# Kernel tuning notes

Measured on AMD Instinct MI355X. Metric: run time of the kernel, lower is better.

## Reference

```python
import jax, jax.numpy as jnp
import numpy as np

EPS_KERNEL = 1e-4   # eps inside softmax_kernel exp
EPS_ATTN = 1e-6     # eps added to k_cumsum in infer_hidden_states
CHUNK = 128         # default chunk_size of infer_hidden_states
HEADS = 8


def softmax_kernel(data, proj, is_query):
    # Performer FAVOR+ softmax kernel feature map.
    dn = data.shape[-1] ** -0.25                 # data normalizer
    ratio = proj.shape[0] ** -0.5
    dd = jnp.einsum('bhnd,jd->bhnj', dn * data, proj)        # [b,h,n,f]
    diag = 0.5 * (dn ** 2) * jnp.sum(data * data, axis=-1, keepdims=True)
    if is_query:
        m = jnp.max(dd, axis=-1, keepdims=True)
    else:
        m = jnp.max(dd)
    return ratio * (jnp.exp(dd - diag - m) + EPS_KERNEL)


def setup_inputs() -> dict:
    key = jax.random.key(0)
    ks = jax.random.split(key, 6)
    b, n, dim, dh, nf = 2, 4096, 512, 64, 256
    sc = dim ** -0.5
    return {
        'x': jax.random.normal(ks[0], (b, n, dim), jnp.float32),
        'Wq': jax.random.normal(ks[1], (dim, dim), jnp.float32) * sc,
        'Wk': jax.random.normal(ks[2], (dim, dim), jnp.float32) * sc,
        'Wv': jax.random.normal(ks[3], (dim, dim), jnp.float32) * sc,
        'Wo': jax.random.normal(ks[4], (dim, dim), jnp.float32) * sc,
        'bo': jnp.zeros((dim,), jnp.float32),
        'proj': jax.random.normal(ks[5], (nf, dh), jnp.float32),
    }


def reference(x, Wq, Wk, Wv, Wo, bo, proj):
    b, n, dim = x.shape
    h = HEADS
    dh = dim // h
    def heads(t):
        return t.reshape(b, n, h, dh).transpose(0, 2, 1, 3)  # [b,h,n,dh]
    q = heads(x @ Wq.T)
    k = heads(x @ Wk.T)
    v = heads(x @ Wv.T)

    # feature maps (post_phi_layerPE=True, pos_emb=None)
    q = softmax_kernel(q, proj, True)    # [b,h,n,f]
    k = softmax_kernel(k, proj, False)   # [b,h,n,f]

    nc = n // CHUNK
    def to_chunks(t):
        f = t.shape[-1]
        return t.reshape(b, h, nc, CHUNK, f).transpose(2, 0, 1, 3, 4)  # [nc,b,h,c,f]
    qc, kc, vc = to_chunks(q), to_chunks(k), to_chunks(v)

    f = q.shape[-1]
    Z0 = jnp.zeros((b, h, 1, f), q.dtype)
    S0 = jnp.zeros((b, h, 1, f, dh), q.dtype)

    def step(carry, qkv):
        Z, S = carry
        qi, ki, vi = qkv                              # [b,h,c,*]
        k_cum = Z + jnp.cumsum(ki, axis=2)            # [b,h,c,f]
        D_inv = 1.0 / jnp.einsum('bhnd,bhnd->bhn', qi, k_cum + EPS_ATTN)
        ctx = jnp.einsum('bhnd,bhne->bhnde', ki, vi)  # [b,h,c,f,dh]
        ctx_cum = S + jnp.cumsum(ctx, axis=2)
        out = jnp.einsum('bhnde,bhnd,bhn->bhne', ctx_cum, qi, D_inv)
        return (k_cum[:, :, -1:], ctx_cum[:, :, -1:]), out

    (Zf, Sf), outs = jax.lax.scan(step, (Z0, S0), (qc, kc, vc))
    # outs: [nc,b,h,c,dh] -> [b,h,n,dh]
    out = outs.transpose(1, 2, 0, 3, 4).reshape(b, h, n, dh)
    out = out.transpose(0, 2, 1, 3).reshape(b, n, h * dh)
    out = out @ Wo.T + bo
    # states: Z=[b,h,f], S=[b,h,f,dh]
    return out, Zf[:, :, 0], Sf[:, :, 0]
```

## Files before the change

kernel.cpp:

```cpp
#include <hip/hip_runtime.h>

typedef unsigned short u16;
typedef unsigned int u32;
typedef __attribute__((ext_vector_type(8))) short bf16x8;
typedef __attribute__((ext_vector_type(4))) float f32x4;

#define LOG2E 1.4426950408889634f

__device__ __forceinline__ u16 f2bf(float f) {
    u32 u = __float_as_uint(f);
    return (u16)((u + 0x7fffu + ((u >> 16) & 1u)) >> 16);
}
__device__ __forceinline__ float bf2f(u16 h) { return __uint_as_float(((u32)h) << 16); }
__device__ __forceinline__ u32 pk(u16 a, u16 b) { return (u32)a | ((u32)b << 16); }
__device__ __forceinline__ int swz(int row, int col, int ld) {
    return ((row * ld + col) * 2) ^ ((row & 7) << 4);
}
__device__ __forceinline__ f32x4 MF(bf16x8 a, bf16x8 b, f32x4 c) {
    return __builtin_amdgcn_mfma_f32_16x16x32_bf16(a, b, c, 0, 0, 0);
}
__device__ __forceinline__ float wave_max(float v) {
    #pragma unroll
    for (int o = 32; o; o >>= 1) v = fmaxf(v, __shfl_xor(v, o));
    return v;
}
__device__ __forceinline__ void gload16(const void* g, void* l) {
    __builtin_amdgcn_global_load_lds(
        (const __attribute__((address_space(1))) void*)g,
        (__attribute__((address_space(3))) void*)l, 16, 0, 0);
}
__device__ __forceinline__ float gmax_decode(const u32* gmaxkey) {
    u32 key = *gmaxkey;
    u32 ub = (key & 0x80000000u) ? (key & 0x7fffffffu) : ~key;
    return __uint_as_float(ub);
}

template<bool ISB>
__global__ __launch_bounds__(256)
void conv_split(const float* __restrict__ src, u16* __restrict__ dst,
                int K, long total4, float scale)
{
    const int K4 = K >> 2;
    for (long i = (long)blockIdx.x * 256 + threadIdx.x; i < total4;
         i += (long)gridDim.x * 256) {
        long row = i / K4;
        int c = (int)(i - row * K4) * 4;
        float4 v = ((const float4*)src)[i];
        float a0 = v.x * scale, a1 = v.y * scale, a2 = v.z * scale, a3 = v.w * scale;
        u16 h0 = f2bf(a0), h1 = f2bf(a1), h2 = f2bf(a2), h3 = f2bf(a3);
        u16 l0 = f2bf(a0 - bf2f(h0)), l1 = f2bf(a1 - bf2f(h1));
        u16 l2 = f2bf(a2 - bf2f(h2)), l3 = f2bf(a3 - bf2f(h3));
        uint2 hh; hh.x = pk(h0, h1); hh.y = pk(h2, h3);
        uint2 ll; ll.x = pk(l0, l1); ll.y = pk(l2, l3);
        u16* d = dst + row * (3L * K) + c;
        *(uint2*)d = hh;
        *(uint2*)(d + (ISB ? 2 * K : K)) = hh;
        *(uint2*)(d + (ISB ? K : 2 * K)) = ll;
    }
}

__global__ __launch_bounds__(256)
void conv_plain(const float* __restrict__ src, u16* __restrict__ dst, long total4)
{
    for (long i = (long)blockIdx.x * 256 + threadIdx.x; i < total4;
         i += (long)gridDim.x * 256) {
        float4 v = ((const float4*)src)[i];
        ushort4 o;
        o.x = f2bf(v.x); o.y = f2bf(v.y); o.z = f2bf(v.z); o.w = f2bf(v.w);
        ((ushort4*)dst)[i] = o;
    }
}

__global__ __launch_bounds__(256)
void conv_w4(const float* __restrict__ Wq, const float* __restrict__ Wk,
             const float* __restrict__ Wv, const float* __restrict__ Wo,
             u16* __restrict__ Wqkvs, u16* __restrict__ Wos)
{
    const int seg = blockIdx.x >> 6;
    const float* src = seg == 0 ? Wq : (seg == 1 ? Wk : (seg == 2 ? Wv : Wo));
    u16* dst = (seg == 3) ? Wos : (Wqkvs + (size_t)seg * 262144);
    long i = (long)(blockIdx.x & 63) * 256 + threadIdx.x;
    for (; i < 65536L; i += 16384L) {
        float4 v = ((const float4*)src)[i];
        ushort4 o;
        o.x = f2bf(v.x); o.y = f2bf(v.y); o.z = f2bf(v.z); o.w = f2bf(v.w);
        ((ushort4*)dst)[i] = o;
    }
}

__global__ __launch_bounds__(256, 3)
void qkv_gemm(const u16* __restrict__ A, const u16* __restrict__ B,
              u16* __restrict__ qs, float* __restrict__ diagb,
              u16* __restrict__ vpl)
{
    __shared__ char smem[34816];
    char* As = smem; char* Bs = smem + 16384;
    const int m0 = blockIdx.x * 128, by = blockIdx.y, n0 = by * 128;
    const int tid = threadIdx.x, lane = tid & 63, wave = tid >> 6;
    const int wm = (wave >> 1) * 64, wn = (wave & 1) * 64;
    const int fr = lane & 15, fk = (lane >> 4) * 8;
    const int lr8 = lane >> 3;
    const int cE = ((lane & 7) ^ lr8) << 3;
    f32x4 acc[4][4] = {};
    for (int k0 = 0; k0 < 512; k0 += 64) {
        #pragma unroll
        for (int t = 0; t < 4; t++) {
            int i = wave * 4 + t;
            int r = (i << 3) + lr8;
            gload16(A + (size_t)(m0 + r) * 512 + k0 + cE, As + (i << 10));
            gload16(B + (size_t)(n0 + r) * 512 + k0 + cE, Bs + (i << 10));
        }
        __syncthreads();
        #pragma unroll
        for (int ks = 0; ks < 2; ks++) {
            bf16x8 af[4], bfv[4];
            #pragma unroll
            for (int mf = 0; mf < 4; mf++)
                af[mf] = *(bf16x8*)(As + swz(wm + mf * 16 + fr, ks * 32 + fk, 64));
            #pragma unroll
            for (int nf = 0; nf < 4; nf++)
                bfv[nf] = *(bf16x8*)(Bs + swz(wn + nf * 16 + fr, ks * 32 + fk, 64));
            #pragma unroll
            for (int mf = 0; mf < 4; mf++)
                #pragma unroll
                for (int nf = 0; nf < 4; nf++)
                    acc[mf][nf] = MF(af[mf], bfv[nf], acc[mf][nf]);
        }
        __syncthreads();
    }
    const float dn = 0.35355339059327373f;
    const int sel = by >> 2;
    float* st = (float*)smem;
    for (int half = 0; half < 2; half++) {
        __syncthreads();
        if ((wave >> 1) == half) {
            #pragma unroll
            for (int mf = 0; mf < 4; mf++) {
                int lr = mf * 16 + (lane >> 4) * 4;
                #pragma unroll
                for (int nf = 0; nf < 4; nf++) {
                    int col = wn + nf * 16 + fr;
                    #pragma unroll
                    for (int r = 0; r < 4; r++)
                        st[(lr + r) * 130 + col] = acc[mf][nf][r];
                }
            }
        }
        __syncthreads();
        int grow = m0 + half * 64 + (tid >> 2);
        if (sel < 2) {
            int hl = (tid >> 1) & 1, e0 = (tid & 1) * 32;
            int h = (by & 3) * 2 + hl;
            alignas(16) u16 hbuf[32], lbuf[32];
            float ss = 0.f;
            #pragma unroll
            for (int q = 0; q < 32; q++) {
                float v = dn * st[(tid >> 2) * 130 + hl * 64 + e0 + q];
                ss += v * v;
                u16 hh = f2bf(v); hbuf[q] = hh; lbuf[q] = f2bf(v - bf2f(hh));
            }
            ss += __shfl_xor(ss, 1);
            if ((tid & 1) == 0)
                diagb[(size_t)sel * 65536 + grow * 8 + h] = 0.5f * LOG2E * ss;
            u16* d = qs + (size_t)sel * 12582912 + (size_t)grow * 1536 + h * 192 + e0;
            #pragma unroll
            for (int q = 0; q < 4; q++) *(uint4*)(d + q * 8) = *(uint4*)&hbuf[q * 8];
            #pragma unroll
            for (int q = 0; q < 4; q++) *(uint4*)(d + 64 + q * 8) = *(uint4*)&hbuf[q * 8];
            #pragma unroll
            for (int q = 0; q < 4; q++) *(uint4*)(d + 128 + q * 8) = *(uint4*)&lbuf[q * 8];
        } else {
            int e0 = (tid & 3) * 32;
            int colbase = (by & 3) * 128 + e0;
            alignas(16) u16 hbuf[32], lbuf[32];
            #pragma unroll
            for (int q = 0; q < 32; q++) {
                float v = st[(tid >> 2) * 130 + e0 + q];
                u16 hh = f2bf(v); hbuf[q] = hh; lbuf[q] = f2bf(v - bf2f(hh));
            }
            u16* dh = vpl + (size_t)grow * 512 + colbase;
            u16* dl = dh + 4194304;
            #pragma unroll
            for (int q = 0; q < 4; q++) *(uint4*)(dh + q * 8) = *(uint4*)&hbuf[q * 8];
            #pragma unroll
            for (int q = 0; q < 4; q++) *(uint4*)(dl + q * 8) = *(uint4*)&lbuf[q * 8];
        }
    }
}

__global__ __launch_bounds__(256, 3)
void dd_gemm(const u16* __restrict__ Aq, const u16* __restrict__ Ak,
             const u16* __restrict__ Bp,
             const float* __restrict__ diagb, u32* __restrict__ gmax,
             u16* __restrict__ phiQ, u16* __restrict__ psiK)
{
    __shared__ char sm_[42240];
    char* As = sm_;
    char* Bs = sm_ + 8192;
    float* red  = (float*)(sm_ + 40960);
    float* srow = (float*)(sm_ + 41984);
    const int isq = (blockIdx.z < 8);
    const int h = isq ? blockIdx.z : (blockIdx.z - 8);
    const int m0 = blockIdx.x * 64;
    const u16* Ag = (isq ? Aq : Ak) + (size_t)m0 * 1536 + h * 192;
    const int tid = threadIdx.x, lane = tid & 63, wave = tid >> 6;
    const int wn = wave * 64;
    const int fr = lane & 15, fk = (lane >> 4) * 8;
    const int lr8 = lane >> 3;
    const int cE = ((lane & 7) ^ lr8) << 3;
    f32x4 acc[4][4] = {};
    for (int k0 = 0; k0 < 192; k0 += 64) {
        #pragma unroll
        for (int t = 0; t < 2; t++) {
            int i = wave * 2 + t;
            int r = (i << 3) + lr8;
            gload16(Ag + (size_t)r * 1536 + k0 + cE, As + (i << 10));
        }
        #pragma unroll
        for (int t = 0; t < 8; t++) {
            int i = wave * 8 + t;
            int r = (i << 3) + lr8;
            gload16(Bp + (size_t)r * 192 + k0 + cE, Bs + (i << 10));
        }
        __syncthreads();
        #pragma unroll
        for (int ks = 0; ks < 2; ks++) {
            bf16x8 af[4], bf4[4];
            #pragma unroll
            for (int mf = 0; mf < 4; mf++)
                af[mf] = *(bf16x8*)(As + swz(mf * 16 + fr, ks * 32 + fk, 64));
            #pragma unroll
            for (int nf = 0; nf < 4; nf++)
                bf4[nf] = *(bf16x8*)(Bs + swz(wn + nf * 16 + fr, ks * 32 + fk, 64));
            #pragma unroll
            for (int mf = 0; mf < 4; mf++)
                #pragma unroll
                for (int nf = 0; nf < 4; nf++)
                    acc[mf][nf] = MF(af[mf], bf4[nf], acc[mf][nf]);
        }
        __syncthreads();
    }

    if (!isq) {
        float mx = -1e30f;
        #pragma unroll
        for (int mf = 0; mf < 4; mf++)
            #pragma unroll
            for (int nf = 0; nf < 4; nf++)
                #pragma unroll
                for (int r = 0; r < 4; r++) mx = fmaxf(mx, acc[mf][nf][r]);
        mx = wave_max(mx);
        __syncthreads();
        if (lane == 0) red[wave] = mx;
        __syncthreads();
        if (tid == 0) {
            float m4 = fmaxf(fmaxf(red[0], red[1]), fmaxf(red[2], red[3]));
            u32 u = __float_as_uint(m4);
            u32 key = (u & 0x80000000u) ? ~u : (u | 0x80000000u);
            atomicMax(gmax, key);
        }
        if (tid < 64)
            srow[tid] = diagb[65536 + (size_t)(m0 + tid) * 8 + h];
    } else {
        float rm[4][4];
        #pragma unroll
        for (int mf = 0; mf < 4; mf++)
            #pragma unroll
            for (int r = 0; r < 4; r++) {
                float m = acc[mf][0][r];
                m = fmaxf(m, acc[mf][1][r]);
                m = fmaxf(m, acc[mf][2][r]);
                m = fmaxf(m, acc[mf][3][r]);
                #pragma unroll
                for (int o = 1; o < 16; o <<= 1) m = fmaxf(m, __shfl_xor(m, o));
                rm[mf][r] = m;
            }
        __syncthreads();
        if ((lane & 15) == 0) {
            #pragma unroll
            for (int mf = 0; mf < 4; mf++)
                #pragma unroll
                for (int r = 0; r < 4; r++)
                    red[(mf * 16 + (lane >> 4) * 4 + r) * 4 + wave] = rm[mf][r];
        }
        __syncthreads();
        if (tid < 64) {
            float m4 = fmaxf(fmaxf(red[tid * 4], red[tid * 4 + 1]),
                             fmaxf(red[tid * 4 + 2], red[tid * 4 + 3]));
            srow[tid] = m4 + diagb[(size_t)(m0 + tid) * 8 + h];
        }
    }
    u16* stg = (u16*)sm_;
    __syncthreads();
    #pragma unroll
    for (int mf = 0; mf < 4; mf++)
        #pragma unroll
        for (int r = 0; r < 4; r++) {
            int row = mf * 16 + (lane >> 4) * 4 + r;
            float s = srow[row];
            #pragma unroll
            for (int nf = 0; nf < 4; nf++) {
                float v = acc[mf][nf][r];
                u16 o = isq ? f2bf(0.0625f * (exp2f(v - s) + 1e-4f))
                            : f2bf(exp2f(v - s));
                stg[row * 264 + wn + nf * 16 + fr] = o;
            }
        }
    __syncthreads();
    {
        int lr = tid >> 2, c0 = (tid & 3) * 64;
        u16* base = isq ? phiQ : psiK;
        u16* dst = base + (size_t)(m0 + lr) * 2048 + h * 256 + c0;
        #pragma unroll
        for (int q = 0; q < 8; q++)
            *(uint4*)(dst + q * 8) = *(uint4*)(stg + lr * 264 + c0 + q * 8);
    }
}

__global__ __launch_bounds__(256)
void transpose_kv(const u16* __restrict__ phiK, u16* __restrict__ phiKT,
                  const u16* __restrict__ vpl, u16* __restrict__ Vt)
{
    __shared__ u16 tr[64 * 136];
    const int isk = (blockIdx.x < 512);
    const int gc = isk ? blockIdx.x : (blockIdx.x - 512);
    const int c = gc & 31, bh = gc >> 5, b = bh >> 3, h = bh & 7;
    const int row0 = b * 4096 + c * 128;
    const int tid = threadIdx.x;
    if (isk) {
        const u16* src = phiK + (size_t)row0 * 2048 + h * 256;
        u16* dst = phiKT + (size_t)gc * 32768;
        for (int f0 = 0; f0 < 256; f0 += 64) {
            #pragma unroll
            for (int j = 0; j < 4; j++) {
                int ci = tid + j * 256; int r = ci >> 3, ff = (ci & 7) * 8;
                bf16x8 w = *(const bf16x8*)(src + (size_t)r * 2048 + f0 + ff);
                #pragma unroll
                for (int q = 0; q < 8; q++) tr[(ff + q) * 136 + r] = (u16)w[q];
            }
            __syncthreads();
            {
                int f = tid >> 2, r0 = (tid & 3) * 32;
                uint4 a0 = *(uint4*)&tr[f * 136 + r0];
                uint4 a1 = *(uint4*)&tr[f * 136 + r0 + 8];
                uint4 a2 = *(uint4*)&tr[f * 136 + r0 + 16];
                uint4 a3 = *(uint4*)&tr[f * 136 + r0 + 24];
                u16* dp = dst + (size_t)(f0 + f) * 128 + r0;
                *(uint4*)dp = a0; *(uint4*)(dp + 8) = a1;
                *(uint4*)(dp + 16) = a2; *(uint4*)(dp + 24) = a3;
            }
            __syncthreads();
        }
    } else {
        u16* dstb = Vt + (size_t)gc * 16384;
        for (int pl = 0; pl < 2; pl++) {
            if (pl) __syncthreads();
            const u16* src = vpl + (size_t)pl * 4194304 + (size_t)row0 * 512 + h * 64;
            #pragma unroll
            for (int j = 0; j < 8; j++) {
                int ci = tid + j * 256; int r = ci >> 4, e = (ci & 15) * 4;
                ushort4 v = *(const ushort4*)(src + (size_t)r * 512 + e);
                tr[(e + 0) * 136 + r] = v.x;
                tr[(e + 1) * 136 + r] = v.y;
                tr[(e + 2) * 136 + r] = v.z;
                tr[(e + 3) * 136 + r] = v.w;
            }
            __syncthreads();
            int e = tid >> 2, r0 = (tid & 3) * 32;
            u16* dst = dstb + pl * 8192;
            #pragma unroll
            for (int q = 0; q < 4; q++) {
                uint4 a = *(uint4*)&tr[e * 136 + r0 + q * 8];
                *(uint4*)(dst + (size_t)e * 128 + r0 + q * 8) = a;
            }
        }
    }
}

__global__ __launch_bounds__(256, 3)
void proj_gemm(const u16* __restrict__ A, const u16* __restrict__ B,
               float* __restrict__ C, const float* __restrict__ bias)
{
    __shared__ char smem[34816];
    char* As = smem; char* Bs = smem + 16384;
    const int m0 = blockIdx.x * 128, n0 = blockIdx.y * 128;
    const int tid = threadIdx.x, lane = tid & 63, wave = tid >> 6;
    const int wm = (wave >> 1) * 64, wn = (wave & 1) * 64;
    const int fr = lane & 15, fk = (lane >> 4) * 8;
    const int lr8 = lane >> 3;
    const int cE = ((lane & 7) ^ lr8) << 3;
    f32x4 acc[4][4] = {};
    for (int k0 = 0; k0 < 512; k0 += 64) {
        #pragma unroll
        for (int t = 0; t < 4; t++) {
            int i = wave * 4 + t;
            int r = (i << 3) + lr8;
            gload16(A + (size_t)(m0 + r) * 512 + k0 + cE, As + (i << 10));
            gload16(B + (size_t)(n0 + r) * 512 + k0 + cE, Bs + (i << 10));
        }
        __syncthreads();
        #pragma unroll
        for (int ks = 0; ks < 2; ks++) {
            bf16x8 af[4], bfv[4];
            #pragma unroll
            for (int mf = 0; mf < 4; mf++)
                af[mf] = *(bf16x8*)(As + swz(wm + mf * 16 + fr, ks * 32 + fk, 64));
            #pragma unroll
            for (int nf = 0; nf < 4; nf++)
                bfv[nf] = *(bf16x8*)(Bs + swz(wn + nf * 16 + fr, ks * 32 + fk, 64));
            #pragma unroll
            for (int mf = 0; mf < 4; mf++)
                #pragma unroll
                for (int nf = 0; nf < 4; nf++)
                    acc[mf][nf] = MF(af[mf], bfv[nf], acc[mf][nf]);
        }
        __syncthreads();
    }
    float* st = (float*)smem;
    for (int half = 0; half < 2; half++) {
        __syncthreads();
        if ((wave >> 1) == half) {
            #pragma unroll
            for (int mf = 0; mf < 4; mf++) {
                int lr = mf * 16 + (lane >> 4) * 4;
                #pragma unroll
                for (int nf = 0; nf < 4; nf++) {
                    int col = wn + nf * 16 + fr;
                    #pragma unroll
                    for (int r = 0; r < 4; r++)
                        st[(lr + r) * 130 + col] = acc[mf][nf][r];
                }
            }
        }
        __syncthreads();
        int lr = tid >> 2, c0 = (tid & 3) * 32;
        int grow = m0 + half * 64 + lr;
        float* dst = C + (size_t)grow * 512 + n0 + c0;
        #pragma unroll
        for (int q = 0; q < 8; q++) {
            float4 v;
            v.x = st[lr * 130 + c0 + q * 4 + 0] + bias[n0 + c0 + q * 4 + 0];
            v.y = st[lr * 130 + c0 + q * 4 + 1] + bias[n0 + c0 + q * 4 + 1];
            v.z = st[lr * 130 + c0 + q * 4 + 2] + bias[n0 + c0 + q * 4 + 2];
            v.w = st[lr * 130 + c0 + q * 4 + 3] + bias[n0 + c0 + q * 4 + 3];
            *(float4*)(dst + q * 4) = v;
        }
    }
}

__global__ __launch_bounds__(256)
void chunk_sums_mfma(const u16* __restrict__ phiKT, const u16* __restrict__ Vt,
                     const u32* __restrict__ gmaxkey,
                     float* __restrict__ sbuf, float* __restrict__ zbuf)
{
    __shared__ char smem[49152];
    __shared__ float vcs[64];
    char* bufA = smem;
    char* bufBh = smem + 32768;
    char* bufBl = smem + 40960;
    const float mg = gmax_decode(gmaxkey);
    const float aF = 0.0625f * exp2f(-mg);
    const float bF = 0.0625f * 1e-4f;
    const int gc = blockIdx.x;
    const u16* Ag = phiKT + (size_t)gc * 32768;
    const u16* Bg = Vt + (size_t)gc * 16384;
    const int tid = threadIdx.x, lane = tid & 63, wave = tid >> 6;
    const int fr = lane & 15, fk = (lane >> 4) * 8;
    const int lr8 = lane >> 3;
    const int cE = ((lane & 7) ^ lr8) << 3;
    {
        float z = 0.f;
        const u16* zp = Ag + (size_t)tid * 128;
        #pragma unroll
        for (int j = 0; j < 16; j++) {
            bf16x8 w = *(const bf16x8*)(zp + j * 8);
            #pragma unroll
            for (int q = 0; q < 8; q++) z += bf2f((u16)w[q]);
        }
        zbuf[(size_t)gc * 256 + tid] = aF * z + bF * 128.0f;
    }
    if (tid < 64) {
        const u16* vh = Bg + (size_t)tid * 128;
        const u16* vl = vh + 8192;
        float s = 0.f;
        #pragma unroll
        for (int j = 0; j < 16; j++) {
            bf16x8 wh = *(const bf16x8*)(vh + j * 8);
            bf16x8 wl = *(const bf16x8*)(vl + j * 8);
            #pragma unroll
            for (int q = 0; q < 8; q++)
                s += bf2f((u16)wh[q]) + bf2f((u16)wl[q]);
        }
        vcs[tid] = s;
    }
    f32x4 acc[4][4] = {};
    for (int kh = 0; kh < 2; kh++) {
        #pragma unroll
        for (int t = 0; t < 8; t++) {
            int i = wave * 8 + t;
            int f = (i << 3) + lr8;
            gload16(Ag + (size_t)f * 128 + kh * 64 + cE, bufA + (i << 10));
        }
        #pragma unroll
        for (int t = 0; t < 2; t++) {
            int i = wave * 2 + t;
            int e = (i << 3) + lr8;
            gload16(Bg + (size_t)e * 128 + kh * 64 + cE, bufBh + (i << 10));
            gload16(Bg + 8192 + (size_t)e * 128 + kh * 64 + cE, bufBl + (i << 10));
        }
        __syncthreads();
        #pragma unroll
        for (int ks = 0; ks < 2; ks++) {
            bf16x8 af[4], bh4[4], bl4[4];
            #pragma unroll
            for (int mf = 0; mf < 4; mf++)
                af[mf] = *(bf16x8*)(bufA + swz(wave * 64 + mf * 16 + fr, ks * 32 + fk, 64));
            #pragma unroll
            for (int nf = 0; nf < 4; nf++) {
                bh4[nf] = *(bf16x8*)(bufBh + swz(nf * 16 + fr, ks * 32 + fk, 64));
                bl4[nf] = *(bf16x8*)(bufBl + swz(nf * 16 + fr, ks * 32 + fk, 64));
            }
            #pragma unroll
            for (int mf = 0; mf < 4; mf++)
                #pragma unroll
                for (int nf = 0; nf < 4; nf++) {
                    acc[mf][nf] = MF(af[mf], bh4[nf], acc[mf][nf]);
                    acc[mf][nf] = MF(af[mf], bl4[nf], acc[mf][nf]);
                }
        }
        __syncthreads();
    }
    #pragma unroll
    for (int mf = 0; mf < 4; mf++) {
        int fb = wave * 64 + mf * 16 + (lane >> 4) * 4;
        #pragma unroll
        for (int nf = 0; nf < 4; nf++) {
            int e = nf * 16 + fr;
            float vb = bF * vcs[e];
            #pragma unroll
            for (int r = 0; r < 4; r++)
                sbuf[(size_t)gc * 16384 + (size_t)(fb + r) * 64 + e] =
                    aF * acc[mf][nf][r] + vb;
        }
    }
}

__global__ __launch_bounds__(256)
void prefix_scan(const float* __restrict__ sbuf, const float* __restrict__ zbuf,
                 u16* __restrict__ SpT, float* __restrict__ Zp,
                 float* __restrict__ outZ, float* __restrict__ outS)
{
    __shared__ float trans[64 * 17];
    const int bh = blockIdx.x >> 4, f0 = (blockIdx.x & 15) * 16;
    const int tid = threadIdx.x;
    const int e_ = tid >> 2, fl = (tid & 3) * 4;
    float run[4] = {0.f, 0.f, 0.f, 0.f};
    float zrun = 0.f;
    for (int c = 0; c < 32; c++) {
        const int gc = bh * 32 + c;
        const float* base = sbuf + (size_t)gc * 16384 + f0 * 64;
        float v[4];
        #pragma unroll
        for (int i = 0; i < 4; i++) v[i] = base[tid + i * 256];
        #pragma unroll
        for (int i = 0; i < 4; i++) {
            int idx = tid + i * 256;
            trans[(idx & 63) * 17 + (idx >> 6)] = run[i];
        }
        float zv = 0.f;
        if (tid < 16) zv = zbuf[(size_t)gc * 256 + f0 + tid];
        __syncthreads();
        {
            alignas(8) u16 hb[4], lb[4];
            #pragma unroll
            for (int q = 0; q < 4; q++) {
                float vv = trans[e_ * 17 + fl + q];
                u16 hh = f2bf(vv); hb[q] = hh; lb[q] = f2bf(vv - bf2f(hh));
            }
            u16* dh = SpT + (size_t)gc * 32768 + e_ * 256 + f0 + fl;
            *(uint2*)dh = *(uint2*)hb;
            *(uint2*)(dh + 16384) = *(uint2*)lb;
        }
        if (tid < 16) { Zp[(size_t)gc * 256 + f0 + tid] = zrun; zrun += zv; }
        #pragma unroll
        for (int i = 0; i < 4; i++) run[i] += v[i];
        __syncthreads();
    }
    #pragma unroll
    for (int i = 0; i < 4; i++)
        outS[(size_t)bh * 16384 + f0 * 64 + tid + i * 256] = run[i];
    if (tid < 16) outZ[bh * 256 + f0 + tid] = zrun;
}

__global__ __launch_bounds__(256)
void chunk_out_mfma(const u16* __restrict__ phiQ, const u16* __restrict__ psiK,
                    const u16* __restrict__ Vt, const u16* __restrict__ SpT,
                    const float* __restrict__ Zp, const u32* __restrict__ gmaxkey,
                    u16* __restrict__ aouts)
{
    extern __shared__ char sm[];
    char* bufQ = sm;
    char* bufK = sm + 16384;
    char* bufA = sm + 32768;
    float* Dl = (float*)(sm + 65536);
    float* Zl = (float*)(sm + 66048);
    float* RowQ = (float*)(sm + 66304);
    const float mg = gmax_decode(gmaxkey);
    const float aF = 0.0625f * exp2f(-mg);
    const float bF = 0.0625f * 1e-4f;
    const int gc = blockIdx.x, c = gc & 31, bh = gc >> 5, b = bh >> 3, h = bh & 7;
    const int row0 = b * 4096 + c * 128;
    const u16* Qg = phiQ + (size_t)row0 * 2048 + h * 256;
    const u16* Kg = psiK + (size_t)row0 * 2048 + h * 256;
    const u16* Vg = Vt + (size_t)gc * 16384;
    const u16* Sg = SpT + (size_t)gc * 32768;
    const float* Zg = Zp + (size_t)gc * 256;
    const int tid = threadIdx.x, lane = tid & 63, wave = tid >> 6;
    const int fr = lane & 15, fk = (lane >> 4) * 8;
    const int dr = tid >> 1, dc = (tid & 1) * 32;
    const int lr8 = lane >> 3;
    const int cE = ((lane & 7) ^ lr8) << 3;

    f32x4 acc2[2][8] = {};
    f32x4 acc1[2][4] = {};
    float dotZ = 0.f, sumQ = 0.f;

    for (int f0 = 0; f0 < 256; f0 += 64) {
        #pragma unroll
        for (int t = 0; t < 4; t++) {
            int i = wave * 4 + t;
            int r = (i << 3) + lr8;
            gload16(Qg + (size_t)r * 2048 + f0 + cE, bufQ + (i << 10));
            gload16(Kg + (size_t)r * 2048 + f0 + cE, bufK + (i << 10));
        }
        #pragma unroll
        for (int t = 0; t < 2; t++) {
            int i = wave * 2 + t;
            int e = (i << 3) + lr8;
            gload16(Sg + (size_t)e * 256 + f0 + cE, bufA + (i << 10));
            gload16(Sg + 16384 + (size_t)e * 256 + f0 + cE, bufA + 8192 + (i << 10));
        }
        if (tid < 64) Zl[tid] = Zg[f0 + tid];
        __syncthreads();
        #pragma unroll
        for (int ks = 0; ks < 2; ks++) {
            bf16x8 af[2];
            af[0] = *(bf16x8*)(bufQ + swz(wave * 32 + fr, ks * 32 + fk, 64));
            af[1] = *(bf16x8*)(bufQ + swz(wave * 32 + 16 + fr, ks * 32 + fk, 64));
            #pragma unroll
            for (int nf = 0; nf < 8; nf++) {
                bf16x8 bv = *(bf16x8*)(bufK + swz(nf * 16 + fr, ks * 32 + fk, 64));
                acc2[0][nf] = MF(af[0], bv, acc2[0][nf]);
                acc2[1][nf] = MF(af[1], bv, acc2[1][nf]);
            }
            #pragma unroll
            for (int nf = 0; nf < 4; nf++) {
                bf16x8 bvh = *(bf16x8*)(bufA + swz(nf * 16 + fr, ks * 32 + fk, 64));
                bf16x8 bvl = *(bf16x8*)(bufA + 8192 + swz(nf * 16 + fr, ks * 32 + fk, 64));
                acc1[0][nf] = MF(af[0], bvh, acc1[0][nf]);
                acc1[1][nf] = MF(af[1], bvh, acc1[1][nf]);
                acc1[0][nf] = MF(af[0], bvl, acc1[0][nf]);
                acc1[1][nf] = MF(af[1], bvl, acc1[1][nf]);
            }
        }
        #pragma unroll
        for (int jj = 0; jj < 4; jj++) {
            bf16x8 qv = *(bf16x8*)(bufQ + swz(dr, dc + jj * 8, 64));
            f32x4 z0 = *(f32x4*)(Zl + dc + jj * 8);
            f32x4 z1 = *(f32x4*)(Zl + dc + jj * 8 + 4);
            #pragma unroll
            for (int q = 0; q < 8; q++) {
                float qf = bf2f((u16)qv[q]);
                sumQ += qf;
                dotZ += qf * (q < 4 ? z0[q] : z1[q - 4]);
            }
        }
        __syncthreads();
    }
    {
        float rq = sumQ + __shfl_xor(sumQ, 1);
        if ((tid & 1) == 0) RowQ[dr] = rq;
    }
    __syncthreads();
    float4 vvh[4];
    #pragma unroll
    for (int j = 0; j < 4; j++) {
        int ci = tid + j * 256; int e = ci >> 4, cc = (ci & 15) * 8;
        vvh[j] = *(const float4*)(Vg + (size_t)e * 128 + cc);
    }
    #pragma unroll
    for (int mf = 0; mf < 2; mf++) {
        int rb = wave * 32 + mf * 16 + (lane >> 4) * 4;
        #pragma unroll
        for (int nf = 0; nf < 8; nf++) {
            int col = nf * 16 + fr;
            #pragma unroll
            for (int r = 0; r < 4; r++) {
                float v = (col <= rb + r) ? (aF * acc2[mf][nf][r] + bF * RowQ[rb + r]) : 0.f;
                *(u16*)(bufA + swz(rb + r, col, 128)) = f2bf(v);
            }
        }
    }
    #pragma unroll
    for (int j = 0; j < 4; j++) {
        int ci = tid + j * 256; int e = ci >> 4, cc = (ci & 15) * 8;
        *(float4*)(bufK + swz(e, cc, 128)) = vvh[j];
    }
    __syncthreads();
    {
        const int dcA = (tid & 1) * 64;
        float rs = 0.f;
        #pragma unroll
        for (int jj = 0; jj < 8; jj++) {
            bf16x8 av = *(bf16x8*)(bufA + swz(dr, dcA + jj * 8, 128));
            #pragma unroll
            for (int q = 0; q < 8; q++) rs += bf2f((u16)av[q]);
        }
        float tot = rs + dotZ + 1e-6f * sumQ;
        tot += __shfl_xor(tot, 1);
        if ((tid & 1) == 0) Dl[dr] = tot;
    }
    #pragma unroll
    for (int ks = 0; ks < 4; ks++) {
        bf16x8 af[2];
        af[0] = *(bf16x8*)(bufA + swz(wave * 32 + fr, ks * 32 + fk, 128));
        af[1] = *(bf16x8*)(bufA + swz(wave * 32 + 16 + fr, ks * 32 + fk, 128));
        #pragma unroll
        for (int nf = 0; nf < 4; nf++) {
            bf16x8 bvh = *(bf16x8*)(bufK + swz(nf * 16 + fr, ks * 32 + fk, 128));
            acc1[0][nf] = MF(af[0], bvh, acc1[0][nf]);
            acc1[1][nf] = MF(af[1], bvh, acc1[1][nf]);
        }
    }
    __syncthreads();
    float* st = (float*)sm;
    #pragma unroll
    for (int mf = 0; mf < 2; mf++) {
        int rb = wave * 32 + mf * 16 + (lane >> 4) * 4;
        #pragma unroll
        for (int r = 0; r < 4; r++) {
            float dinv = 1.f / Dl[rb + r];
            #pragma unroll
            for (int nf = 0; nf < 4; nf++)
                st[(rb + r) * 65 + nf * 16 + fr] = acc1[mf][nf][r] * dinv;
        }
    }
    __syncthreads();
    {
        int lr = tid >> 1, e0 = (tid & 1) * 32;
        alignas(16) u16 hb[32];
        #pragma unroll
        for (int q = 0; q < 32; q++) hb[q] = f2bf(st[lr * 65 + e0 + q]);
        u16* d = aouts + (size_t)(row0 + lr) * 512 + h * 64 + e0;
        #pragma unroll
        for (int q = 0; q < 4; q++) *(uint4*)(d + q * 8) = *(uint4*)&hb[q * 8];
    }
}

extern "C" void kernel_launch(void* const* d_in, const int* in_sizes, int n_in,
                              void* d_out, int out_size, void* d_ws, size_t ws_size,
                              hipStream_t stream)
{
    const float* x    = (const float*)d_in[0];
    const float* Wq   = (const float*)d_in[1];
    const float* Wk   = (const float*)d_in[2];
    const float* Wv   = (const float*)d_in[3];
    const float* Wo   = (const float*)d_in[4];
    const float* bo   = (const float*)d_in[5];
    const float* proj = (const float*)d_in[6];
    float* out = (float*)d_out;
    float* ws = (float*)d_ws;

    u16*   vpl   = (u16*)ws;
    float* diagb = ws + 4194304;
    u16*   phi   = (u16*)(ws + 12582912);
    u16*   Vtb   = (u16*)(ws + 37748736);
    float* sbuf  = ws + 41943040;
    u16*   qs    = (u16*)(ws + 41943040);
    u16*   phiKT = (u16*)(ws + 50331648);
    u16*   SpT   = (u16*)(ws + 50331648);
    u16*   xs    = (u16*)(ws + 58720256);
    u16*   aouts = xs;
    u16*   Wqkvs = (u16*)(ws + 65011712);
    float* zbuf  = ws + 65142784;
    float* Zp    = ws + 65273856;
    u32*   gmax  = (u32*)(ws + 65404928);
    u16*   Wos   = (u16*)(ws + 66191360);
    u16*   projs = (u16*)(ws + 66584576);

    float* outO = out;
    float* outZ = out + 4194304;
    float* outS = out + 4198400;

    dim3 blk(256);

    conv_plain<<<1024, blk, 0, stream>>>(x, xs, 1048576L);
    conv_w4<<<256, blk, 0, stream>>>(Wq, Wk, Wv, Wo, Wqkvs, Wos);
    conv_split<true ><<<16, blk, 0, stream>>>(proj, projs, 64, 4096L, LOG2E);
    qkv_gemm<<<dim3(64, 12), blk, 0, stream>>>(xs, Wqkvs, qs, diagb, vpl);
    hipMemsetAsync(gmax, 0, 4, stream);
    const u16* ksplit = qs + 12582912;
    u16* psiK = phi + (size_t)8192 * 2048;
    dd_gemm<<<dim3(128, 1, 16), blk, 0, stream>>>(qs, ksplit, projs, diagb, gmax,
                                                  phi, psiK);
    transpose_kv<<<1024, blk, 0, stream>>>(psiK, phiKT, vpl, Vtb);
    chunk_sums_mfma<<<512, blk, 0, stream>>>(phiKT, Vtb, gmax, sbuf, zbuf);
    prefix_scan<<<256, blk, 0, stream>>>(sbuf, zbuf, SpT, Zp, outZ, outS);
    hipFuncSetAttribute((const void*)chunk_out_mfma,
                        hipFuncAttributeMaxDynamicSharedMemorySize, 66816);
    chunk_out_mfma<<<512, blk, 66816, stream>>>(phi, psiK, Vtb, SpT, Zp, gmax, aouts);
    proj_gemm<<<dim3(64, 4), blk, 0, stream>>>(aouts, Wos, outO, bo);
}
```

Before: 215.4 us.

## Write V transposed directly from QKV GEMM epilogue and drop V transpose pass

```diff
diff --git a/kernel.cpp b/kernel.cpp
--- a/kernel.cpp
+++ b/kernel.cpp
@@ -1,4 +1,5 @@
 #include <hip/hip_runtime.h>
+#include <hip/hip_bf16.h>
 
 typedef unsigned short u16;
 typedef unsigned int u32;
@@ -8,8 +9,8 @@
 #define LOG2E 1.4426950408889634f
 
 __device__ __forceinline__ u16 f2bf(float f) {
-    u32 u = __float_as_uint(f);
-    return (u16)((u + 0x7fffu + ((u >> 16) & 1u)) >> 16);
+    __hip_bfloat16 h = __float2bfloat16(f);
+    u16 u; __builtin_memcpy(&u, &h, 2); return u;
 }
 __device__ __forceinline__ float bf2f(u16 h) { return __uint_as_float(((u32)h) << 16); }
 __device__ __forceinline__ u32 pk(u16 a, u16 b) { return (u32)a | ((u32)b << 16); }
@@ -91,7 +92,7 @@
 __global__ __launch_bounds__(256, 3)
 void qkv_gemm(const u16* __restrict__ A, const u16* __restrict__ B,
               u16* __restrict__ qs, float* __restrict__ diagb,
-              u16* __restrict__ vpl)
+              u16* __restrict__ Vtb)
 {
     __shared__ char smem[34816];
     char* As = smem; char* Bs = smem + 16384;
@@ -147,8 +148,8 @@
             }
         }
         __syncthreads();
-        int grow = m0 + half * 64 + (tid >> 2);
         if (sel < 2) {
+            int grow = m0 + half * 64 + (tid >> 2);
             int hl = (tid >> 1) & 1, e0 = (tid & 1) * 32;
             int h = (by & 3) * 2 + hl;
             alignas(16) u16 hbuf[32], lbuf[32];
@@ -170,16 +171,20 @@
             #pragma unroll
             for (int q = 0; q < 4; q++) *(uint4*)(d + 128 + q * 8) = *(uint4*)&lbuf[q * 8];
         } else {
-            int e0 = (tid & 3) * 32;
-            int colbase = (by & 3) * 128 + e0;
+            const int bb = blockIdx.x >> 5, cc2 = blockIdx.x & 31;
+            int e_full = tid >> 1;
+            int h_local = e_full >> 6;
+            int e = e_full & 63;
+            int rhalf = (tid & 1) * 32;
+            int gc = (bb * 8 + (by & 3) * 2 + h_local) * 32 + cc2;
             alignas(16) u16 hbuf[32], lbuf[32];
             #pragma unroll
             for (int q = 0; q < 32; q++) {
-                float v = st[(tid >> 2) * 130 + e0 + q];
+                float v = st[(rhalf + q) * 130 + h_local * 64 + e];
                 u16 hh = f2bf(v); hbuf[q] = hh; lbuf[q] = f2bf(v - bf2f(hh));
             }
-            u16* dh = vpl + (size_t)grow * 512 + colbase;
-            u16* dl = dh + 4194304;
+            u16* dh = Vtb + (size_t)gc * 16384 + (size_t)e * 128 + half * 64 + rhalf;
+            u16* dl = dh + 8192;
             #pragma unroll
             for (int q = 0; q < 4; q++) *(uint4*)(dh + q * 8) = *(uint4*)&hbuf[q * 8];
             #pragma unroll
@@ -318,62 +323,34 @@
 }
 
 __global__ __launch_bounds__(256)
-void transpose_kv(const u16* __restrict__ phiK, u16* __restrict__ phiKT,
-                  const u16* __restrict__ vpl, u16* __restrict__ Vt)
+void transpose_k(const u16* __restrict__ phiK, u16* __restrict__ phiKT)
 {
     __shared__ u16 tr[64 * 136];
-    const int isk = (blockIdx.x < 512);
-    const int gc = isk ? blockIdx.x : (blockIdx.x - 512);
-    const int c = gc & 31, bh = gc >> 5, b = bh >> 3, h = bh & 7;
+    const int gc = blockIdx.x, c = gc & 31, bh = gc >> 5, b = bh >> 3, h = bh & 7;
     const int row0 = b * 4096 + c * 128;
+    const u16* src = phiK + (size_t)row0 * 2048 + h * 256;
+    u16* dst = phiKT + (size_t)gc * 32768;
     const int tid = threadIdx.x;
-    if (isk) {
-        const u16* src = phiK + (size_t)row0 * 2048 + h * 256;
-        u16* dst = phiKT + (size_t)gc * 32768;
-        for (int f0 = 0; f0 < 256; f0 += 64) {
-            #pragma unroll
-            for (int j = 0; j < 4; j++) {
-                int ci = tid + j * 256; int r = ci >> 3, ff = (ci & 7) * 8;
-                bf16x8 w = *(const bf16x8*)(src + (size_t)r * 2048 + f0 + ff);
-                #pragma unroll
-                for (int q = 0; q < 8; q++) tr[(ff + q) * 136 + r] = (u16)w[q];
-            }
-            __syncthreads();
-            {
-                int f = tid >> 2, r0 = (tid & 3) * 32;
-                uint4 a0 = *(uint4*)&tr[f * 136 + r0];
-                uint4 a1 = *(uint4*)&tr[f * 136 + r0 + 8];
-                uint4 a2 = *(uint4*)&tr[f * 136 + r0 + 16];
-                uint4 a3 = *(uint4*)&tr[f * 136 + r0 + 24];
-                u16* dp = dst + (size_t)(f0 + f) * 128 + r0;
-                *(uint4*)dp = a0; *(uint4*)(dp + 8) = a1;
-                *(uint4*)(dp + 16) = a2; *(uint4*)(dp + 24) = a3;
-            }
-            __syncthreads();
-        }
-    } else {
-        u16* dstb = Vt + (size_t)gc * 16384;
-        for (int pl = 0; pl < 2; pl++) {
-            if (pl) __syncthreads();
-            const u16* src = vpl + (size_t)pl * 4194304 + (size_t)row0 * 512 + h * 64;
-            #pragma unroll
-            for (int j = 0; j < 8; j++) {
-                int ci = tid + j * 256; int r = ci >> 4, e = (ci & 15) * 4;
-                ushort4 v = *(const ushort4*)(src + (size_t)r * 512 + e);
-                tr[(e + 0) * 136 + r] = v.x;
-                tr[(e + 1) * 136 + r] = v.y;
-                tr[(e + 2) * 136 + r] = v.z;
-                tr[(e + 3) * 136 + r] = v.w;
-            }
-            __syncthreads();
-            int e = tid >> 2, r0 = (tid & 3) * 32;
-            u16* dst = dstb + pl * 8192;
-            #pragma unroll
-            for (int q = 0; q < 4; q++) {
-                uint4 a = *(uint4*)&tr[e * 136 + r0 + q * 8];
-                *(uint4*)(dst + (size_t)e * 128 + r0 + q * 8) = a;
-            }
-        }
+    for (int f0 = 0; f0 < 256; f0 += 64) {
+        #pragma unroll
+        for (int j = 0; j < 4; j++) {
+            int ci = tid + j * 256; int r = ci >> 3, ff = (ci & 7) * 8;
+            bf16x8 w = *(const bf16x8*)(src + (size_t)r * 2048 + f0 + ff);
+            #pragma unroll
+            for (int q = 0; q < 8; q++) tr[(ff + q) * 136 + r] = (u16)w[q];
+        }
+        __syncthreads();
+        {
+            int f = tid >> 2, r0 = (tid & 3) * 32;
+            uint4 a0 = *(uint4*)&tr[f * 136 + r0];
+            uint4 a1 = *(uint4*)&tr[f * 136 + r0 + 8];
+            uint4 a2 = *(uint4*)&tr[f * 136 + r0 + 16];
+            uint4 a3 = *(uint4*)&tr[f * 136 + r0 + 24];
+            u16* dp = dst + (size_t)(f0 + f) * 128 + r0;
+            *(uint4*)dp = a0; *(uint4*)(dp + 8) = a1;
+            *(uint4*)(dp + 16) = a2; *(uint4*)(dp + 24) = a3;
+        }
+        __syncthreads();
     }
 }
 
@@ -771,7 +748,6 @@
     float* out = (float*)d_out;
     float* ws = (float*)d_ws;
 
-    u16*   vpl   = (u16*)ws;
     float* diagb = ws + 4194304;
     u16*   phi   = (u16*)(ws + 12582912);
     u16*   Vtb   = (u16*)(ws + 37748736);
@@ -797,13 +773,13 @@
     conv_plain<<<1024, blk, 0, stream>>>(x, xs, 1048576L);
     conv_w4<<<256, blk, 0, stream>>>(Wq, Wk, Wv, Wo, Wqkvs, Wos);
     conv_split<true ><<<16, blk, 0, stream>>>(proj, projs, 64, 4096L, LOG2E);
-    qkv_gemm<<<dim3(64, 12), blk, 0, stream>>>(xs, Wqkvs, qs, diagb, vpl);
+    qkv_gemm<<<dim3(64, 12), blk, 0, stream>>>(xs, Wqkvs, qs, diagb, Vtb);
     hipMemsetAsync(gmax, 0, 4, stream);
     const u16* ksplit = qs + 12582912;
     u16* psiK = phi + (size_t)8192 * 2048;
     dd_gemm<<<dim3(128, 1, 16), blk, 0, stream>>>(qs, ksplit, projs, diagb, gmax,
                                                   phi, psiK);
-    transpose_kv<<<1024, blk, 0, stream>>>(psiK, phiKT, vpl, Vtb);
+    transpose_k<<<512, blk, 0, stream>>>(psiK, phiKT);
     chunk_sums_mfma<<<512, blk, 0, stream>>>(phiKT, Vtb, gmax, sbuf, zbuf);
     prefix_scan<<<256, blk, 0, stream>>>(sbuf, zbuf, SpT, Zp, outZ, outS);
     hipFuncSetAttribute((const void*)chunk_out_mfma,
```

Result: faster. 208.4 us (-3.2%).
